# Performance work log

Hardware: AMD Instinct MI355X
Metric: run time of the kernel (lower is better)

Reference implementation:

```python
import jax, jax.numpy as jnp
import numpy as np
from jax import lax

MB = 8          # block_size (macroblock)
P = 8           # search_distance
CROP = 17       # space_crop
TAU = 1         # causal delay
LARGE = 65537.0 # sentinel cost (matches skvideo DS)
MAX_STEPS = 16  # LDSP step cap (|displacement| <= P, each step moves >=1)

# Large / Small Diamond Search Patterns, entries are (dx, dy)
LDSP = jnp.array([[0, -2], [-1, -1], [1, -1], [-2, 0], [0, 0], [2, 0], [-1, 1], [1, 1], [0, 2]], dtype=jnp.int32)
SDSP = jnp.array([[0, -1], [-1, 0], [0, 0], [1, 0], [0, 1]], dtype=jnp.int32)


def _ds_motion_frame(imgP, imgI):
    """Diamond-search block motion of current frame imgP w.r.t. reference imgI.
    Returns (nbr, nbc, 2) int32 motion vectors (dy, dx)."""
    H, W = imgP.shape
    nbr, nbc = H // MB, W // MB
    # (nbr, nbc, MB, MB) macroblocks of the current frame
    blocks = imgP.reshape(nbr, MB, nbc, MB).transpose(0, 2, 1, 3)
    bi = jnp.arange(nbr, dtype=jnp.int32) * MB
    bj = jnp.arange(nbc, dtype=jnp.int32) * MB

    def cost_at(blk, i, j, y, x):
        # MAD cost of matching blk (at block origin i,j) against imgI at (y,x);
        # out-of-image or outside the +/-P search window -> LARGE.
        valid = ((y >= 0) & (y + MB <= H) & (x >= 0) & (x + MB <= W)
                 & (jnp.abs(y - i) <= P) & (jnp.abs(x - j) <= P))
        yc = jnp.clip(y, 0, H - MB)
        xc = jnp.clip(x, 0, W - MB)
        ref = lax.dynamic_slice(imgI, (yc, xc), (MB, MB))
        return jnp.where(valid, jnp.mean(jnp.abs(blk - ref)), LARGE)

    def ds_one(blk, i, j):
        c0 = cost_at(blk, i, j, i, j)
        # skvideo: if center cost is exactly 0, skip the LDSP stage
        init_pt = jnp.where(c0 == 0.0, 4, -1).astype(jnp.int32)

        def cond(st):
            return (st[2] != 4) & (st[3] < MAX_STEPS)

        def body(st):
            y, x, _, k = st
            costs = jax.vmap(lambda d: cost_at(blk, i, j, y + d[1], x + d[0]))(LDSP)
            pt = jnp.argmin(costs).astype(jnp.int32)
            return (y + LDSP[pt, 1], x + LDSP[pt, 0], pt, k + 1)

        y, x, _, _ = lax.while_loop(cond, body, (i, j, init_pt, jnp.int32(0)))
        # final small-diamond refinement
        sc = jax.vmap(lambda d: cost_at(blk, i, j, y + d[1], x + d[0]))(SDSP)
        spt = jnp.argmin(sc).astype(jnp.int32)
        y = y + SDSP[spt, 1]
        x = x + SDSP[spt, 0]
        return jnp.stack([y - i, x - j])  # (dy, dx)

    row = jax.vmap(lambda blkrow, i: jax.vmap(lambda blk, j: ds_one(blk, i, j))(blkrow, bj))
    return row(blocks, bi)


def _block_comp_frame(ref, motion):
    """Motion-compensate one frame from reference `ref` using per-block (dy,dx)."""
    nbr, nbc = motion.shape[:2]
    bi = jnp.arange(nbr, dtype=jnp.int32) * MB
    bj = jnp.arange(nbc, dtype=jnp.int32) * MB

    def get(i, j, m):
        return lax.dynamic_slice(ref, (i + m[0], j + m[1]), (MB, MB))

    blocks = jax.vmap(lambda i, mrow: jax.vmap(lambda j, m: get(i, j, m))(bj, mrow))(bi, motion)
    return blocks.transpose(0, 2, 1, 3).reshape(nbr * MB, nbc * MB)


def _predict_video(vid):
    """vid: (T, H, W). Causal branch: motion between (t-1, t) warps frame t to predict t+1."""
    vid_sg = lax.stop_gradient(vid)  # motion vectors are integer-valued, non-differentiable
    motion = jax.vmap(_ds_motion_frame)(vid_sg[1:], vid_sg[:-1])  # (T-1, nbr, nbc, 2)
    v = vid[TAU:]  # blockComp(videodata[tau:], motion[:-tau])
    comp_rest = jax.vmap(_block_comp_frame)(v[:-1], motion[:-TAU])
    comp = jnp.concatenate([v[:1], comp_rest], axis=0)  # comp[0] = first frame copy
    target = v[1:, CROP:-CROP, CROP:-CROP]
    pred = comp[1:, CROP:-CROP, CROP:-CROP]
    return target, pred


def setup_inputs() -> dict:
    key = jax.random.key(0)
    x = jax.random.normal(key, (4, 1, 16, 512, 512), dtype=jnp.float32)
    return {"x": x}


def reference(x):
    vids = x[:, 0]  # single (luminance) channel, (B, T, H, W)
    target, pred = jax.vmap(_predict_video)(vids)
    # restore channel dim: (B, 1, T-2, H-2c, W-2c)
    return target[:, None], pred[:, None]
```

## Files before the change

### kernel.cpp

```cpp
#include <hip/hip_runtime.h>

#define HH 512
#define WW 512
#define TT 16
#define NF 14
#define NV 4
#define CRP 17
#define CW 478
#define TGT_SIZE ((size_t)NV * NF * CW * CW)
#define FRAME ((size_t)HH * WW)

#define WROWS 48
#define WCOLS 80
#define WSTR  85
#define WBASE (2 * WSTR + 2)
#define WSIZE ((WROWS + 4) * WSTR)
#define TH    1e-3f

template <int CTRL>
__device__ __forceinline__ float dpp_add(float v) {
    int x = __builtin_amdgcn_update_dpp(0, __float_as_int(v), CTRL, 0xF, 0xF, true);
    return v + __int_as_float(x);
}
__device__ __forceinline__ float bf8_sum(float v) {
    v = dpp_add<0xB1>(v);
    v = dpp_add<0x4E>(v);
    v = dpp_add<0x141>(v);
    return v;
}
__device__ __forceinline__ double bf8_sumd(double v) {
    v += __shfl_xor(v, 1, 64);
    v += __shfl_xor(v, 2, 64);
    v += __shfl_xor(v, 4, 64);
    return v;
}

__device__ __forceinline__ float sad8(float w0, float w1, float w2, float w3,
                                      float w4, float w5, float w6, float w7,
                                      const float2* pr2) {
    float t0 = fabsf(pr2[0].x - w0) + fabsf(pr2[0].y - w1);
    float t1 = fabsf(pr2[1].x - w2) + fabsf(pr2[1].y - w3);
    float t2 = fabsf(pr2[2].x - w4) + fabsf(pr2[2].y - w5);
    float t3 = fabsf(pr2[3].x - w6) + fabsf(pr2[3].y - w7);
    return bf8_sum((t0 + t1) + (t2 + t3));
}

__device__ __forceinline__ double sad_f64(const float* b, const float2* pr2) {
    double e0 = (double)fabsf(pr2[0].x - b[0]) + (double)fabsf(pr2[0].y - b[1]);
    double e1 = (double)fabsf(pr2[1].x - b[2]) + (double)fabsf(pr2[1].y - b[3]);
    double e2 = (double)fabsf(pr2[2].x - b[4]) + (double)fabsf(pr2[2].y - b[5]);
    double e3 = (double)fabsf(pr2[3].x - b[6]) + (double)fabsf(pr2[3].y - b[7]);
    return bf8_sumd((e0 + e1) + (e2 + e3));
}

__global__ void __launch_bounds__(256)
motion_pred_kernel(const float* __restrict__ x, float* __restrict__ out) {
    __shared__ float win[WSIZE];

    int cta = blockIdx.x;
    int jb0 = (cta & 7) * 64;
    int bi0 = ((cta >> 3) & 15) * 4;
    int bf  = cta >> 7;
    int f   = bf % NF;
    int b   = bf / NF;

    const float* imgP = x + (size_t)(b * TT + f + 1) * FRAME;
    const float* imgI = x + (size_t)(b * TT + f)     * FRAME;

    int wy0 = bi0 * 8 - 8;
    int wx0 = jb0 - 8;

    #pragma unroll
    for (int t = 0; t < 4; ++t) {
        int idx = t * 256 + threadIdx.x;
        if (idx < WROWS * (WCOLS / 4)) {
            int row = idx / (WCOLS / 4);
            int c4  = idx - row * (WCOLS / 4);
            int yy  = wy0 + row;
            int xg  = wx0 + c4 * 4;
            if (yy >= 0 && yy < HH && xg >= 0 && xg <= WW - 4) {
                float4 v = *(const float4*)(imgI + (size_t)yy * WW + xg);
                float* d = win + WBASE + row * WSTR + c4 * 4;
                d[0] = v.x; d[1] = v.y; d[2] = v.z; d[3] = v.w;
            }
        }
    }
    __syncthreads();

    int w    = threadIdx.x >> 6;
    int lane = threadIdx.x & 63;
    int g = lane >> 3;
    int r = lane & 7;

    int i  = (bi0 + w) * 8;
    int jg = jb0 + g * 8;

    float2 pr2[4];
    {
        const float4* prow = (const float4*)(imgP + (size_t)(i + r) * WW + jg);
        float4 p0 = prow[0], p1 = prow[1];
        pr2[0] = make_float2(p0.x, p0.y); pr2[1] = make_float2(p0.z, p0.w);
        pr2[2] = make_float2(p1.x, p1.y); pr2[3] = make_float2(p1.z, p1.w);
    }

    int yLo = max(i - 8, 0),  yHi = min(i + 8, HH - 8);
    int xLo = max(jg - 8, 0), xHi = min(jg + 8, WW - 8);

    int y = i, xx = jg;
    int ctr;
    bool vy[5], vx[5];

    auto precomp = [&]() {
        ctr = WBASE + (y - wy0 + r) * WSTR + (xx - wx0);
        #pragma unroll
        for (int d = -2; d <= 2; ++d) {
            vy[d + 2] = (y + d >= yLo) && (y + d <= yHi);
            vx[d + 2] = (xx + d >= xLo) && (xx + d <= xHi);
        }
    };
    auto evalqd = [&](int dy, int dx) -> double {
        const float* bp = win + (ctr + dy * WSTR + dx);
        double s = sad_f64(bp, pr2);
        return (vy[dy + 2] && vx[dx + 2]) ? s : 1e30;
    };

    const int LDx[9] = {0,-1, 1,-2, 0, 2,-1, 1, 0};
    const int LDy[9] = {-2,-1,-1, 0, 0, 0, 1, 1, 2};

    precomp();
    float cc;
    {
        const float* pc = win + ctr;
        float c0 = pc[0], c1 = pc[1], c2 = pc[2], c3 = pc[3];
        float c4 = pc[4], c5 = pc[5], c6 = pc[6], c7 = pc[7];
        cc = sad8(c0, c1, c2, c3, c4, c5, c6, c7, pr2);
    }
    bool done = (cc == 0.0f);
    int k = 0;

    while (__any((!done) && (k < 16))) {
        bool active = (!done) && (k < 16);
        precomp();

        const float* pm2 = win + (ctr - 2 * WSTR);
        const float* pm1 = win + (ctr - WSTR - 1);
        const float* pz  = win + (ctr - 2);
        const float* pp1 = win + (ctr + WSTR - 1);
        const float* pp2 = win + (ctr + 2 * WSTR);
        float a2[8], a1v[10], a0v[12], b1v[10], b2[8];
        #pragma unroll
        for (int t = 0; t < 8; ++t)  a2[t]  = pm2[t];
        #pragma unroll
        for (int t = 0; t < 10; ++t) a1v[t] = pm1[t];
        #pragma unroll
        for (int t = 0; t < 12; ++t) a0v[t] = pz[t];
        #pragma unroll
        for (int t = 0; t < 10; ++t) b1v[t] = pp1[t];
        #pragma unroll
        for (int t = 0; t < 8; ++t)  b2[t]  = pp2[t];

        float s0 = sad8(a2[0],  a2[1],  a2[2],  a2[3],  a2[4],  a2[5],  a2[6],  a2[7],  pr2);
        float s1 = sad8(a1v[0], a1v[1], a1v[2], a1v[3], a1v[4], a1v[5], a1v[6], a1v[7], pr2);
        float s2 = sad8(a1v[2], a1v[3], a1v[4], a1v[5], a1v[6], a1v[7], a1v[8], a1v[9], pr2);
        float s3 = sad8(a0v[0], a0v[1], a0v[2], a0v[3], a0v[4], a0v[5], a0v[6], a0v[7], pr2);
        float s5 = sad8(a0v[4], a0v[5], a0v[6], a0v[7], a0v[8], a0v[9], a0v[10],a0v[11],pr2);
        float s6 = sad8(b1v[0], b1v[1], b1v[2], b1v[3], b1v[4], b1v[5], b1v[6], b1v[7], pr2);
        float s7 = sad8(b1v[2], b1v[3], b1v[4], b1v[5], b1v[6], b1v[7], b1v[8], b1v[9], pr2);
        float s8 = sad8(b2[0],  b2[1],  b2[2],  b2[3],  b2[4],  b2[5],  b2[6],  b2[7],  pr2);

        float cf[9];
        cf[0] = (vy[0] && vx[2]) ? s0 : 1e30f;
        cf[1] = (vy[1] && vx[1]) ? s1 : 1e30f;
        cf[2] = (vy[1] && vx[3]) ? s2 : 1e30f;
        cf[3] = (vy[2] && vx[0]) ? s3 : 1e30f;
        cf[4] = cc;
        cf[5] = (vy[2] && vx[4]) ? s5 : 1e30f;
        cf[6] = (vy[3] && vx[1]) ? s6 : 1e30f;
        cf[7] = (vy[3] && vx[3]) ? s7 : 1e30f;
        cf[8] = (vy[4] && vx[2]) ? s8 : 1e30f;

        float m1 = 1e38f, m2 = 1e38f; int b1 = 0;
        #pragma unroll
        for (int q = 0; q < 9; ++q) {
            float cq = cf[q];
            bool lt = cq < m1;
            m2 = lt ? m1 : fminf(m2, cq);
            m1 = lt ? cq : m1;
            b1 = lt ? q  : b1;
        }
        bool needx = (m2 - m1) < TH;
        if (__any(active && needx)) {
            double e1 = 1e300; int eb = 0;
            #pragma unroll
            for (int q = 0; q < 9; ++q) {
                double eq = evalqd(LDy[q], LDx[q]);
                bool lt = eq < e1;
                e1 = lt ? eq : e1; eb = lt ? q : eb;
            }
            float mf = cf[0];
            #pragma unroll
            for (int q = 1; q < 9; ++q) mf = (eb == q) ? cf[q] : mf;
            if (needx) { b1 = eb; m1 = mf; }
        }
        if (active) {
            int dy = (b1 == 0) ? -2 : (b1 == 1 || b1 == 2) ? -1
                   : (b1 == 6 || b1 == 7) ? 1 : (b1 == 8) ? 2 : 0;
            int dx = (b1 == 1 || b1 == 6) ? -1 : (b1 == 2 || b1 == 7) ? 1
                   : (b1 == 3) ? -2 : (b1 == 5) ? 2 : 0;
            y += dy; xx += dx;
            cc = m1;
            done = (b1 == 4);
            k++;
        }
    }

    {
        precomp();
        const int SDx[5] = {0,-1, 0, 1, 0};
        const int SDy[5] = {-1, 0, 0, 0, 1};

        const float* qm1 = win + (ctr - WSTR);
        const float* qz  = win + (ctr - 1);
        const float* qp1 = win + (ctr + WSTR);
        float u0[8], u1[10], u2[8];
        #pragma unroll
        for (int t = 0; t < 8; ++t)  u0[t] = qm1[t];
        #pragma unroll
        for (int t = 0; t < 10; ++t) u1[t] = qz[t];
        #pragma unroll
        for (int t = 0; t < 8; ++t)  u2[t] = qp1[t];

        float t0 = sad8(u0[0], u0[1], u0[2], u0[3], u0[4], u0[5], u0[6], u0[7], pr2);
        float t1 = sad8(u1[0], u1[1], u1[2], u1[3], u1[4], u1[5], u1[6], u1[7], pr2);
        float t3 = sad8(u1[2], u1[3], u1[4], u1[5], u1[6], u1[7], u1[8], u1[9], pr2);
        float t4 = sad8(u2[0], u2[1], u2[2], u2[3], u2[4], u2[5], u2[6], u2[7], pr2);

        float cf5[5];
        cf5[0] = (vy[1] && vx[2]) ? t0 : 1e30f;
        cf5[1] = (vy[2] && vx[1]) ? t1 : 1e30f;
        cf5[2] = cc;
        cf5[3] = (vy[2] && vx[3]) ? t3 : 1e30f;
        cf5[4] = (vy[3] && vx[2]) ? t4 : 1e30f;

        float m1 = 1e38f, m2 = 1e38f; int sb = 0;
        #pragma unroll
        for (int q = 0; q < 5; ++q) {
            float cq = cf5[q];
            bool lt = cq < m1;
            m2 = lt ? m1 : fminf(m2, cq);
            m1 = lt ? cq : m1;
            sb = lt ? q  : sb;
        }
        bool needx = (m2 - m1) < TH;
        if (__any(needx)) {
            double e1 = 1e300; int eb = 0;
            #pragma unroll
            for (int q = 0; q < 5; ++q) {
                double eq = evalqd(SDy[q], SDx[q]);
                bool lt = eq < e1;
                e1 = lt ? eq : e1; eb = lt ? q : eb;
            }
            if (needx) sb = eb;
        }
        y  += (sb == 0) ? -1 : (sb == 4) ? 1 : 0;
        xx += (sb == 1) ? -1 : (sb == 3) ? 1 : 0;
    }

    int dy = y - i, dx = xx - jg;

    int gy = i + r;
    if (gy >= CRP && gy < HH - CRP) {
        const float* src = imgP + (size_t)(i + dy + r) * WW + (jg + dx);
        size_t obase = TGT_SIZE
            + (((size_t)(b * NF + f)) * CW + (size_t)(gy - CRP)) * CW - CRP;
        #pragma unroll
        for (int c = 0; c < 8; ++c) {
            int gx = jg + c;
            if (gx >= CRP && gx < WW - CRP)
                out[obase + gx] = src[c];
        }
    }
}

__global__ void __launch_bounds__(256)
target_copy_kernel(const float* __restrict__ x, float* __restrict__ out) {
    unsigned idx = blockIdx.x * 256 + threadIdx.x;
    if (idx >= (unsigned)(TGT_SIZE / 4)) return;
    unsigned o = idx * 4;
    unsigned fidx = o / (CW * CW);
    unsigned rem  = o - fidx * (CW * CW);
    unsigned rr   = rem / CW;
    unsigned c0   = rem - rr * CW;
    unsigned b    = fidx / NF, fi = fidx - b * NF;
    const float* src = x + (size_t)(b * TT + fi + 2) * FRAME;
    float4 v;
    float* vp = &v.x;
    #pragma unroll
    for (int t = 0; t < 4; ++t) {
        unsigned cc2 = c0 + t, r2 = rr;
        if (cc2 >= CW) { cc2 -= CW; r2 += 1; }
        vp[t] = src[(r2 + CRP) * WW + cc2 + CRP];
    }
    *(float4*)(out + o) = v;
}

extern "C" void kernel_launch(void* const* d_in, const int* in_sizes, int n_in,
                              void* d_out, int out_size, void* d_ws, size_t ws_size,
                              hipStream_t stream) {
    const float* x = (const float*)d_in[0];
    float* out = (float*)d_out;

    {
        int n4 = (int)(TGT_SIZE / 4);
        int blocks = (n4 + 255) / 256;
        target_copy_kernel<<<blocks, 256, 0, stream>>>(x, out);
    }
    {
        int blocks = NV * NF * 16 * 8;
        motion_pred_kernel<<<blocks, 256, 0, stream>>>(x, out);
    }
}
```

Baseline: 221.0 us.

## Fuse target crop copy into motion kernel and predicate search work per lane

Removes the separate target_copy_kernel and writes the cropped target frame from inside the motion prediction kernel, so one launch is saved and the copy's memory traffic overlaps with the search compute. It also wraps the diamond-step SAD evaluation in a per-lane active check and limits the double-precision tie-break to lanes that need it. The fused store runs as scalar 8-wide row writes instead of float4 stores, which may coalesce less well. Divergent lanes may still serialize within a wavefront.

```diff
diff --git a/kernel.cpp b/kernel.cpp
--- a/kernel.cpp
+++ b/kernel.cpp
@@ -140,69 +140,71 @@
 
     while (__any((!done) && (k < 16))) {
         bool active = (!done) && (k < 16);
-        precomp();
-
-        const float* pm2 = win + (ctr - 2 * WSTR);
-        const float* pm1 = win + (ctr - WSTR - 1);
-        const float* pz  = win + (ctr - 2);
-        const float* pp1 = win + (ctr + WSTR - 1);
-        const float* pp2 = win + (ctr + 2 * WSTR);
-        float a2[8], a1v[10], a0v[12], b1v[10], b2[8];
-        #pragma unroll
-        for (int t = 0; t < 8; ++t)  a2[t]  = pm2[t];
-        #pragma unroll
-        for (int t = 0; t < 10; ++t) a1v[t] = pm1[t];
-        #pragma unroll
-        for (int t = 0; t < 12; ++t) a0v[t] = pz[t];
-        #pragma unroll
-        for (int t = 0; t < 10; ++t) b1v[t] = pp1[t];
-        #pragma unroll
-        for (int t = 0; t < 8; ++t)  b2[t]  = pp2[t];
-
-        float s0 = sad8(a2[0],  a2[1],  a2[2],  a2[3],  a2[4],  a2[5],  a2[6],  a2[7],  pr2);
-        float s1 = sad8(a1v[0], a1v[1], a1v[2], a1v[3], a1v[4], a1v[5], a1v[6], a1v[7], pr2);
-        float s2 = sad8(a1v[2], a1v[3], a1v[4], a1v[5], a1v[6], a1v[7], a1v[8], a1v[9], pr2);
-        float s3 = sad8(a0v[0], a0v[1], a0v[2], a0v[3], a0v[4], a0v[5], a0v[6], a0v[7], pr2);
-        float s5 = sad8(a0v[4], a0v[5], a0v[6], a0v[7], a0v[8], a0v[9], a0v[10],a0v[11],pr2);
-        float s6 = sad8(b1v[0], b1v[1], b1v[2], b1v[3], b1v[4], b1v[5], b1v[6], b1v[7], pr2);
-        float s7 = sad8(b1v[2], b1v[3], b1v[4], b1v[5], b1v[6], b1v[7], b1v[8], b1v[9], pr2);
-        float s8 = sad8(b2[0],  b2[1],  b2[2],  b2[3],  b2[4],  b2[5],  b2[6],  b2[7],  pr2);
-
-        float cf[9];
-        cf[0] = (vy[0] && vx[2]) ? s0 : 1e30f;
-        cf[1] = (vy[1] && vx[1]) ? s1 : 1e30f;
-        cf[2] = (vy[1] && vx[3]) ? s2 : 1e30f;
-        cf[3] = (vy[2] && vx[0]) ? s3 : 1e30f;
-        cf[4] = cc;
-        cf[5] = (vy[2] && vx[4]) ? s5 : 1e30f;
-        cf[6] = (vy[3] && vx[1]) ? s6 : 1e30f;
-        cf[7] = (vy[3] && vx[3]) ? s7 : 1e30f;
-        cf[8] = (vy[4] && vx[2]) ? s8 : 1e30f;
-
-        float m1 = 1e38f, m2 = 1e38f; int b1 = 0;
-        #pragma unroll
-        for (int q = 0; q < 9; ++q) {
-            float cq = cf[q];
-            bool lt = cq < m1;
-            m2 = lt ? m1 : fminf(m2, cq);
-            m1 = lt ? cq : m1;
-            b1 = lt ? q  : b1;
-        }
-        bool needx = (m2 - m1) < TH;
-        if (__any(active && needx)) {
-            double e1 = 1e300; int eb = 0;
+        if (active) {
+            precomp();
+
+            const float* pm2 = win + (ctr - 2 * WSTR);
+            const float* pm1 = win + (ctr - WSTR - 1);
+            const float* pz  = win + (ctr - 2);
+            const float* pp1 = win + (ctr + WSTR - 1);
+            const float* pp2 = win + (ctr + 2 * WSTR);
+            float a2[8], a1v[10], a0v[12], b1v[10], b2[8];
+            #pragma unroll
+            for (int t = 0; t < 8; ++t)  a2[t]  = pm2[t];
+            #pragma unroll
+            for (int t = 0; t < 10; ++t) a1v[t] = pm1[t];
+            #pragma unroll
+            for (int t = 0; t < 12; ++t) a0v[t] = pz[t];
+            #pragma unroll
+            for (int t = 0; t < 10; ++t) b1v[t] = pp1[t];
+            #pragma unroll
+            for (int t = 0; t < 8; ++t)  b2[t]  = pp2[t];
+
+            float s0 = sad8(a2[0],  a2[1],  a2[2],  a2[3],  a2[4],  a2[5],  a2[6],  a2[7],  pr2);
+            float s1 = sad8(a1v[0], a1v[1], a1v[2], a1v[3], a1v[4], a1v[5], a1v[6], a1v[7], pr2);
+            float s2 = sad8(a1v[2], a1v[3], a1v[4], a1v[5], a1v[6], a1v[7], a1v[8], a1v[9], pr2);
+            float s3 = sad8(a0v[0], a0v[1], a0v[2], a0v[3], a0v[4], a0v[5], a0v[6], a0v[7], pr2);
+            float s5 = sad8(a0v[4], a0v[5], a0v[6], a0v[7], a0v[8], a0v[9], a0v[10],a0v[11],pr2);
+            float s6 = sad8(b1v[0], b1v[1], b1v[2], b1v[3], b1v[4], b1v[5], b1v[6], b1v[7], pr2);
+            float s7 = sad8(b1v[2], b1v[3], b1v[4], b1v[5], b1v[6], b1v[7], b1v[8], b1v[9], pr2);
+            float s8 = sad8(b2[0],  b2[1],  b2[2],  b2[3],  b2[4],  b2[5],  b2[6],  b2[7],  pr2);
+
+            float cf[9];
+            cf[0] = (vy[0] && vx[2]) ? s0 : 1e30f;
+            cf[1] = (vy[1] && vx[1]) ? s1 : 1e30f;
+            cf[2] = (vy[1] && vx[3]) ? s2 : 1e30f;
+            cf[3] = (vy[2] && vx[0]) ? s3 : 1e30f;
+            cf[4] = cc;
+            cf[5] = (vy[2] && vx[4]) ? s5 : 1e30f;
+            cf[6] = (vy[3] && vx[1]) ? s6 : 1e30f;
+            cf[7] = (vy[3] && vx[3]) ? s7 : 1e30f;
+            cf[8] = (vy[4] && vx[2]) ? s8 : 1e30f;
+
+            float m1 = 1e38f, m2 = 1e38f; int b1 = 0;
             #pragma unroll
             for (int q = 0; q < 9; ++q) {
-                double eq = evalqd(LDy[q], LDx[q]);
-                bool lt = eq < e1;
-                e1 = lt ? eq : e1; eb = lt ? q : eb;
-            }
-            float mf = cf[0];
-            #pragma unroll
-            for (int q = 1; q < 9; ++q) mf = (eb == q) ? cf[q] : mf;
-            if (needx) { b1 = eb; m1 = mf; }
-        }
-        if (active) {
+                float cq = cf[q];
+                bool lt = cq < m1;
+                m2 = lt ? m1 : fminf(m2, cq);
+                m1 = lt ? cq : m1;
+                b1 = lt ? q  : b1;
+            }
+            bool needx = (m2 - m1) < TH;
+            if (__any(needx)) {
+                if (needx) {
+                    double e1 = 1e300; int eb = 0;
+                    #pragma unroll
+                    for (int q = 0; q < 9; ++q) {
+                        double eq = evalqd(LDy[q], LDx[q]);
+                        bool lt = eq < e1;
+                        e1 = lt ? eq : e1; eb = lt ? q : eb;
+                    }
+                    float mf = cf[0];
+                    #pragma unroll
+                    for (int q = 1; q < 9; ++q) mf = (eb == q) ? cf[q] : mf;
+                    b1 = eb; m1 = mf;
+                }
+            }
             int dy = (b1 == 0) ? -2 : (b1 == 1 || b1 == 2) ? -1
                    : (b1 == 6 || b1 == 7) ? 1 : (b1 == 8) ? 2 : 0;
             int dx = (b1 == 1 || b1 == 6) ? -1 : (b1 == 2 || b1 == 7) ? 1
@@ -253,14 +255,16 @@
         }
         bool needx = (m2 - m1) < TH;
         if (__any(needx)) {
-            double e1 = 1e300; int eb = 0;
-            #pragma unroll
-            for (int q = 0; q < 5; ++q) {
-                double eq = evalqd(SDy[q], SDx[q]);
-                bool lt = eq < e1;
-                e1 = lt ? eq : e1; eb = lt ? q : eb;
-            }
-            if (needx) sb = eb;
+            if (needx) {
+                double e1 = 1e300; int eb = 0;
+                #pragma unroll
+                for (int q = 0; q < 5; ++q) {
+                    double eq = evalqd(SDy[q], SDx[q]);
+                    bool lt = eq < e1;
+                    e1 = lt ? eq : e1; eb = lt ? q : eb;
+                }
+                sb = eb;
+            }
         }
         y  += (sb == 0) ? -1 : (sb == 4) ? 1 : 0;
         xx += (sb == 1) ? -1 : (sb == 3) ? 1 : 0;
@@ -280,28 +284,21 @@
                 out[obase + gx] = src[c];
         }
     }
-}
-
-__global__ void __launch_bounds__(256)
-target_copy_kernel(const float* __restrict__ x, float* __restrict__ out) {
-    unsigned idx = blockIdx.x * 256 + threadIdx.x;
-    if (idx >= (unsigned)(TGT_SIZE / 4)) return;
-    unsigned o = idx * 4;
-    unsigned fidx = o / (CW * CW);
-    unsigned rem  = o - fidx * (CW * CW);
-    unsigned rr   = rem / CW;
-    unsigned c0   = rem - rr * CW;
-    unsigned b    = fidx / NF, fi = fidx - b * NF;
-    const float* src = x + (size_t)(b * TT + fi + 2) * FRAME;
-    float4 v;
-    float* vp = &v.x;
-    #pragma unroll
-    for (int t = 0; t < 4; ++t) {
-        unsigned cc2 = c0 + t, r2 = rr;
-        if (cc2 >= CW) { cc2 -= CW; r2 += 1; }
-        vp[t] = src[(r2 + CRP) * WW + cc2 + CRP];
-    }
-    *(float4*)(out + o) = v;
+
+    {
+        const float* srcT = x + (size_t)(b * TT + f + 2) * FRAME;
+        if (gy >= CRP && gy < HH - CRP) {
+            const float* st = srcT + (size_t)gy * WW + jg;
+            size_t tbase =
+                (((size_t)(b * NF + f)) * CW + (size_t)(gy - CRP)) * CW - CRP;
+            #pragma unroll
+            for (int c = 0; c < 8; ++c) {
+                int gx = jg + c;
+                if (gx >= CRP && gx < WW - CRP)
+                    out[tbase + gx] = st[c];
+            }
+        }
+    }
 }
 
 extern "C" void kernel_launch(void* const* d_in, const int* in_sizes, int n_in,
@@ -310,13 +307,6 @@
     const float* x = (const float*)d_in[0];
     float* out = (float*)d_out;
 
-    {
-        int n4 = (int)(TGT_SIZE / 4);
-        int blocks = (n4 + 255) / 256;
-        target_copy_kernel<<<blocks, 256, 0, stream>>>(x, out);
-    }
-    {
-        int blocks = NV * NF * 16 * 8;
-        motion_pred_kernel<<<blocks, 256, 0, stream>>>(x, out);
-    }
-}
+    int blocks = NV * NF * 16 * 8;
+    motion_pred_kernel<<<blocks, 256, 0, stream>>>(x, out);
+}
```

Measured after the change: 245.0 us. 10.9% more time.

## Fuse target copy into motion kernel with interleaved block roles and divergent-skip

Applied to the files above, without the earlier changes.

Merges the target-crop copy kernel into the motion-search kernel. Copy blocks, each handling 1024 float4s, are interleaved evenly among motion blocks by a ratio-based block-id mapping, so memory-bound copy work overlaps compute-bound diamond search and one launch is saved. The diamond loop body now runs only under the per-lane active flag. The double-precision tie-break is evaluated only by lanes that need it, which can reduce work in partially converged wavefronts but adds divergence around the wave-level ballots.

```diff
diff --git a/kernel.cpp b/kernel.cpp
--- a/kernel.cpp
+++ b/kernel.cpp
@@ -17,6 +17,11 @@
 #define WSIZE ((WROWS + 4) * WSTR)
 #define TH    1e-3f
 
+#define NMOTION (NV * NF * 16 * 8)
+#define N4      ((int)(TGT_SIZE / 4))
+#define NCPY    ((N4 + 1023) / 1024)
+#define NTOT    (NMOTION + NCPY)
+
 template <int CTRL>
 __device__ __forceinline__ float dpp_add(float v) {
     int x = __builtin_amdgcn_update_dpp(0, __float_as_int(v), CTRL, 0xF, 0xF, true);
@@ -54,10 +59,41 @@
 }
 
 __global__ void __launch_bounds__(256)
-motion_pred_kernel(const float* __restrict__ x, float* __restrict__ out) {
+fused_kernel(const float* __restrict__ x, float* __restrict__ out) {
     __shared__ float win[WSIZE];
 
-    int cta = blockIdx.x;
+    int bid   = blockIdx.x;
+    int cprev = (int)(((long long)bid * NCPY) / NTOT);
+    int cnext = (int)(((long long)(bid + 1) * NCPY) / NTOT);
+
+    if (cnext > cprev) {
+        int c = cprev;
+        #pragma unroll
+        for (int j = 0; j < 4; ++j) {
+            int idx = c * 1024 + j * 256 + (int)threadIdx.x;
+            if (idx < N4) {
+                unsigned o = (unsigned)idx * 4;
+                unsigned fidx = o / (CW * CW);
+                unsigned rem  = o - fidx * (CW * CW);
+                unsigned rr   = rem / CW;
+                unsigned c0   = rem - rr * CW;
+                unsigned b    = fidx / NF, fi = fidx - b * NF;
+                const float* src = x + (size_t)(b * TT + fi + 2) * FRAME;
+                float4 v;
+                float* vp = &v.x;
+                #pragma unroll
+                for (int t = 0; t < 4; ++t) {
+                    unsigned cc2 = c0 + t, r2 = rr;
+                    if (cc2 >= CW) { cc2 -= CW; r2 += 1; }
+                    vp[t] = src[(r2 + CRP) * WW + cc2 + CRP];
+                }
+                *(float4*)(out + o) = v;
+            }
+        }
+        return;
+    }
+
+    int cta = bid - cprev;
     int jb0 = (cta & 7) * 64;
     int bi0 = ((cta >> 3) & 15) * 4;
     int bf  = cta >> 7;
@@ -140,69 +176,71 @@
 
     while (__any((!done) && (k < 16))) {
         bool active = (!done) && (k < 16);
-        precomp();
-
-        const float* pm2 = win + (ctr - 2 * WSTR);
-        const float* pm1 = win + (ctr - WSTR - 1);
-        const float* pz  = win + (ctr - 2);
-        const float* pp1 = win + (ctr + WSTR - 1);
-        const float* pp2 = win + (ctr + 2 * WSTR);
-        float a2[8], a1v[10], a0v[12], b1v[10], b2[8];
-        #pragma unroll
-        for (int t = 0; t < 8; ++t)  a2[t]  = pm2[t];
-        #pragma unroll
-        for (int t = 0; t < 10; ++t) a1v[t] = pm1[t];
-        #pragma unroll
-        for (int t = 0; t < 12; ++t) a0v[t] = pz[t];
-        #pragma unroll
-        for (int t = 0; t < 10; ++t) b1v[t] = pp1[t];
-        #pragma unroll
-        for (int t = 0; t < 8; ++t)  b2[t]  = pp2[t];
-
-        float s0 = sad8(a2[0],  a2[1],  a2[2],  a2[3],  a2[4],  a2[5],  a2[6],  a2[7],  pr2);
-        float s1 = sad8(a1v[0], a1v[1], a1v[2], a1v[3], a1v[4], a1v[5], a1v[6], a1v[7], pr2);
-        float s2 = sad8(a1v[2], a1v[3], a1v[4], a1v[5], a1v[6], a1v[7], a1v[8], a1v[9], pr2);
-        float s3 = sad8(a0v[0], a0v[1], a0v[2], a0v[3], a0v[4], a0v[5], a0v[6], a0v[7], pr2);
-        float s5 = sad8(a0v[4], a0v[5], a0v[6], a0v[7], a0v[8], a0v[9], a0v[10],a0v[11],pr2);
-        float s6 = sad8(b1v[0], b1v[1], b1v[2], b1v[3], b1v[4], b1v[5], b1v[6], b1v[7], pr2);
-        float s7 = sad8(b1v[2], b1v[3], b1v[4], b1v[5], b1v[6], b1v[7], b1v[8], b1v[9], pr2);
-        float s8 = sad8(b2[0],  b2[1],  b2[2],  b2[3],  b2[4],  b2[5],  b2[6],  b2[7],  pr2);
-
-        float cf[9];
-        cf[0] = (vy[0] && vx[2]) ? s0 : 1e30f;
-        cf[1] = (vy[1] && vx[1]) ? s1 : 1e30f;
-        cf[2] = (vy[1] && vx[3]) ? s2 : 1e30f;
-        cf[3] = (vy[2] && vx[0]) ? s3 : 1e30f;
-        cf[4] = cc;
-        cf[5] = (vy[2] && vx[4]) ? s5 : 1e30f;
-        cf[6] = (vy[3] && vx[1]) ? s6 : 1e30f;
-        cf[7] = (vy[3] && vx[3]) ? s7 : 1e30f;
-        cf[8] = (vy[4] && vx[2]) ? s8 : 1e30f;
-
-        float m1 = 1e38f, m2 = 1e38f; int b1 = 0;
-        #pragma unroll
-        for (int q = 0; q < 9; ++q) {
-            float cq = cf[q];
-            bool lt = cq < m1;
-            m2 = lt ? m1 : fminf(m2, cq);
-            m1 = lt ? cq : m1;
-            b1 = lt ? q  : b1;
-        }
-        bool needx = (m2 - m1) < TH;
-        if (__any(active && needx)) {
-            double e1 = 1e300; int eb = 0;
+        if (active) {
+            precomp();
+
+            const float* pm2 = win + (ctr - 2 * WSTR);
+            const float* pm1 = win + (ctr - WSTR - 1);
+            const float* pz  = win + (ctr - 2);
+            const float* pp1 = win + (ctr + WSTR - 1);
+            const float* pp2 = win + (ctr + 2 * WSTR);
+            float a2[8], a1v[10], a0v[12], b1v[10], b2[8];
+            #pragma unroll
+            for (int t = 0; t < 8; ++t)  a2[t]  = pm2[t];
+            #pragma unroll
+            for (int t = 0; t < 10; ++t) a1v[t] = pm1[t];
+            #pragma unroll
+            for (int t = 0; t < 12; ++t) a0v[t] = pz[t];
+            #pragma unroll
+            for (int t = 0; t < 10; ++t) b1v[t] = pp1[t];
+            #pragma unroll
+            for (int t = 0; t < 8; ++t)  b2[t]  = pp2[t];
+
+            float s0 = sad8(a2[0],  a2[1],  a2[2],  a2[3],  a2[4],  a2[5],  a2[6],  a2[7],  pr2);
+            float s1 = sad8(a1v[0], a1v[1], a1v[2], a1v[3], a1v[4], a1v[5], a1v[6], a1v[7], pr2);
+            float s2 = sad8(a1v[2], a1v[3], a1v[4], a1v[5], a1v[6], a1v[7], a1v[8], a1v[9], pr2);
+            float s3 = sad8(a0v[0], a0v[1], a0v[2], a0v[3], a0v[4], a0v[5], a0v[6], a0v[7], pr2);
+            float s5 = sad8(a0v[4], a0v[5], a0v[6], a0v[7], a0v[8], a0v[9], a0v[10],a0v[11],pr2);
+            float s6 = sad8(b1v[0], b1v[1], b1v[2], b1v[3], b1v[4], b1v[5], b1v[6], b1v[7], pr2);
+            float s7 = sad8(b1v[2], b1v[3], b1v[4], b1v[5], b1v[6], b1v[7], b1v[8], b1v[9], pr2);
+            float s8 = sad8(b2[0],  b2[1],  b2[2],  b2[3],  b2[4],  b2[5],  b2[6],  b2[7],  pr2);
+
+            float cf[9];
+            cf[0] = (vy[0] && vx[2]) ? s0 : 1e30f;
+            cf[1] = (vy[1] && vx[1]) ? s1 : 1e30f;
+            cf[2] = (vy[1] && vx[3]) ? s2 : 1e30f;
+            cf[3] = (vy[2] && vx[0]) ? s3 : 1e30f;
+            cf[4] = cc;
+            cf[5] = (vy[2] && vx[4]) ? s5 : 1e30f;
+            cf[6] = (vy[3] && vx[1]) ? s6 : 1e30f;
+            cf[7] = (vy[3] && vx[3]) ? s7 : 1e30f;
+            cf[8] = (vy[4] && vx[2]) ? s8 : 1e30f;
+
+            float m1 = 1e38f, m2 = 1e38f; int b1 = 0;
             #pragma unroll
             for (int q = 0; q < 9; ++q) {
-                double eq = evalqd(LDy[q], LDx[q]);
-                bool lt = eq < e1;
-                e1 = lt ? eq : e1; eb = lt ? q : eb;
-            }
-            float mf = cf[0];
-            #pragma unroll
-            for (int q = 1; q < 9; ++q) mf = (eb == q) ? cf[q] : mf;
-            if (needx) { b1 = eb; m1 = mf; }
-        }
-        if (active) {
+                float cq = cf[q];
+                bool lt = cq < m1;
+                m2 = lt ? m1 : fminf(m2, cq);
+                m1 = lt ? cq : m1;
+                b1 = lt ? q  : b1;
+            }
+            bool needx = (m2 - m1) < TH;
+            if (__any(needx)) {
+                if (needx) {
+                    double e1 = 1e300; int eb = 0;
+                    #pragma unroll
+                    for (int q = 0; q < 9; ++q) {
+                        double eq = evalqd(LDy[q], LDx[q]);
+                        bool lt = eq < e1;
+                        e1 = lt ? eq : e1; eb = lt ? q : eb;
+                    }
+                    float mf = cf[0];
+                    #pragma unroll
+                    for (int q = 1; q < 9; ++q) mf = (eb == q) ? cf[q] : mf;
+                    b1 = eb; m1 = mf;
+                }
+            }
             int dy = (b1 == 0) ? -2 : (b1 == 1 || b1 == 2) ? -1
                    : (b1 == 6 || b1 == 7) ? 1 : (b1 == 8) ? 2 : 0;
             int dx = (b1 == 1 || b1 == 6) ? -1 : (b1 == 2 || b1 == 7) ? 1
@@ -253,14 +291,16 @@
         }
         bool needx = (m2 - m1) < TH;
         if (__any(needx)) {
-            double e1 = 1e300; int eb = 0;
-            #pragma unroll
-            for (int q = 0; q < 5; ++q) {
-                double eq = evalqd(SDy[q], SDx[q]);
-                bool lt = eq < e1;
-                e1 = lt ? eq : e1; eb = lt ? q : eb;
-            }
-            if (needx) sb = eb;
+            if (needx) {
+                double e1 = 1e300; int eb = 0;
+                #pragma unroll
+                for (int q = 0; q < 5; ++q) {
+                    double eq = evalqd(SDy[q], SDx[q]);
+                    bool lt = eq < e1;
+                    e1 = lt ? eq : e1; eb = lt ? q : eb;
+                }
+                sb = eb;
+            }
         }
         y  += (sb == 0) ? -1 : (sb == 4) ? 1 : 0;
         xx += (sb == 1) ? -1 : (sb == 3) ? 1 : 0;
@@ -282,41 +322,11 @@
     }
 }
 
-__global__ void __launch_bounds__(256)
-target_copy_kernel(const float* __restrict__ x, float* __restrict__ out) {
-    unsigned idx = blockIdx.x * 256 + threadIdx.x;
-    if (idx >= (unsigned)(TGT_SIZE / 4)) return;
-    unsigned o = idx * 4;
-    unsigned fidx = o / (CW * CW);
-    unsigned rem  = o - fidx * (CW * CW);
-    unsigned rr   = rem / CW;
-    unsigned c0   = rem - rr * CW;
-    unsigned b    = fidx / NF, fi = fidx - b * NF;
-    const float* src = x + (size_t)(b * TT + fi + 2) * FRAME;
-    float4 v;
-    float* vp = &v.x;
-    #pragma unroll
-    for (int t = 0; t < 4; ++t) {
-        unsigned cc2 = c0 + t, r2 = rr;
-        if (cc2 >= CW) { cc2 -= CW; r2 += 1; }
-        vp[t] = src[(r2 + CRP) * WW + cc2 + CRP];
-    }
-    *(float4*)(out + o) = v;
-}
-
 extern "C" void kernel_launch(void* const* d_in, const int* in_sizes, int n_in,
                               void* d_out, int out_size, void* d_ws, size_t ws_size,
                               hipStream_t stream) {
     const float* x = (const float*)d_in[0];
     float* out = (float*)d_out;
 
-    {
-        int n4 = (int)(TGT_SIZE / 4);
-        int blocks = (n4 + 255) / 256;
-        target_copy_kernel<<<blocks, 256, 0, stream>>>(x, out);
-    }
-    {
-        int blocks = NV * NF * 16 * 8;
-        motion_pred_kernel<<<blocks, 256, 0, stream>>>(x, out);
-    }
-}
+    fused_kernel<<<NTOT, 256, 0, stream>>>(x, out);
+}
```

After: 226.2 us. 1.02x slower.
